# Kernel optimization log

Hardware: AMD Instinct MI355X
Metric: run time of the kernel (lower is better)

## Reference

```python
import jax, jax.numpy as jnp
import numpy as np

N_EMBD = 1024
HEAD_SIZE = 64
T = 8192
LN_EPS = 1e-5


def _layer_norm(x, gamma, beta):
    mu = jnp.mean(x, axis=-1, keepdims=True)
    var = jnp.mean(jnp.square(x - mu), axis=-1, keepdims=True)
    return (x - mu) * jax.lax.rsqrt(var + LN_EPS) * gamma + beta


def setup_inputs() -> dict:
    key = jax.random.key(0)
    ks = jax.random.split(key, 10)
    s_in = 1.0 / np.sqrt(N_EMBD)
    s_hs = 1.0 / np.sqrt(HEAD_SIZE)
    s_ff = 1.0 / np.sqrt(4 * N_EMBD)
    return {
        "x": jax.random.normal(ks[0], (T, N_EMBD), dtype=jnp.float32),
        "Wk": jax.random.uniform(ks[1], (N_EMBD, HEAD_SIZE), jnp.float32, -s_in, s_in),
        "Wq": jax.random.uniform(ks[2], (N_EMBD, HEAD_SIZE), jnp.float32, -s_in, s_in),
        "Wv": jax.random.uniform(ks[3], (N_EMBD, HEAD_SIZE), jnp.float32, -s_in, s_in),
        "Wp": jax.random.uniform(ks[4], (HEAD_SIZE, N_EMBD), jnp.float32, -s_hs, s_hs),
        "W1": jax.random.uniform(ks[5], (N_EMBD, 4 * N_EMBD), jnp.float32, -s_in, s_in),
        "b1": jax.random.uniform(ks[6], (4 * N_EMBD,), jnp.float32, -s_in, s_in),
        "W2": jax.random.uniform(ks[7], (4 * N_EMBD, N_EMBD), jnp.float32, -s_ff, s_ff),
        "b2": jax.random.uniform(ks[8], (N_EMBD,), jnp.float32, -s_ff, s_ff),
        "g1": jnp.ones((N_EMBD,), jnp.float32),
        "be1": jnp.zeros((N_EMBD,), jnp.float32),
        "g2": jnp.ones((N_EMBD,), jnp.float32),
        "be2": jnp.zeros((N_EMBD,), jnp.float32),
    }


def reference(x, Wk, Wq, Wv, Wp, W1, b1, W2, b2, g1, be1, g2, be2):
    Tn = x.shape[0]
    k = x @ Wk            # (T, hs)
    q = x @ Wq            # (T, hs)
    v = x @ Wv            # (T, hs)
    wei = (q @ k.T) * (HEAD_SIZE ** -0.5)       # (T, T)
    causal = jnp.tril(jnp.ones((Tn, Tn), dtype=bool))
    wei = jnp.where(causal, wei, -jnp.inf)
    wei = jax.nn.softmax(wei, axis=-1)
    attn = (wei @ v) @ Wp                        # (T, n_embd)
    x1 = _layer_norm(x + attn, g1, be1)
    y = jax.nn.relu(x1 @ W1 + b1) @ W2 + b2      # FFN
    return _layer_norm(x1 + y, g2, be2)
```

## Files before the change

kernel.cpp:

```cpp
#include <hip/hip_runtime.h>
#include <hip/hip_bf16.h>

#define T_SEQ 8192
#define NE 1024
#define FF 4096

typedef __bf16 bf16_t;
typedef __bf16 bf16x8 __attribute__((ext_vector_type(8)));
typedef __bf16 bf16x4 __attribute__((ext_vector_type(4)));
typedef float f32x4 __attribute__((ext_vector_type(4)));

__device__ __forceinline__ void gll16(const void* g, void* l) {
    __builtin_amdgcn_global_load_lds(
        (const __attribute__((address_space(1))) void*)g,
        (__attribute__((address_space(3))) void*)l, 16, 0, 0);
}

__global__ __launch_bounds__(256) void cast_f32_bf16(const float* __restrict__ in,
                                                     bf16_t* __restrict__ out, int n4) {
    int i = blockIdx.x * 256 + threadIdx.x;
    if (i >= n4) return;
    float4 v = ((const float4*)in)[i];
    bf16x4 h;
    h[0] = (bf16_t)v.x; h[1] = (bf16_t)v.y; h[2] = (bf16_t)v.z; h[3] = (bf16_t)v.w;
    ((bf16x4*)out)[i] = h;
}

__global__ __launch_bounds__(256) void build_wkqv(const float* __restrict__ Wk,
                                                  const float* __restrict__ Wq,
                                                  const float* __restrict__ Wv,
                                                  bf16_t* __restrict__ out) {
    int idx = blockIdx.x * 256 + threadIdx.x;
    int n  = idx >> 10;
    int kk = idx & 1023;
    float v = 0.f;
    if (n < 64)       v = Wk[kk * 64 + n];
    else if (n < 128) v = Wq[kk * 64 + (n - 64)] * 0.125f;
    else if (n < 192) v = Wv[kk * 64 + (n - 128)];
    out[idx] = (bf16_t)v;
}

__global__ __launch_bounds__(256) void tcast(const float* __restrict__ in,
                                             bf16_t* __restrict__ out, int R, int C) {
    __shared__ bf16_t tl[64][66];
    const int bc = blockIdx.x << 6, br = blockIdx.y << 6;
    const int tx = threadIdx.x & 63, ty = threadIdx.x >> 6;
#pragma unroll
    for (int j = 0; j < 16; ++j) {
        const int r = ty + j * 4;
        tl[r][tx] = (bf16_t)in[(size_t)(br + r) * C + bc + tx];
    }
    __syncthreads();
#pragma unroll
    for (int j = 0; j < 16; ++j) {
        const int r = ty + j * 4;
        out[(size_t)(bc + r) * R + br + tx] = tl[tx][r];
    }
}

template <int EPI>
__global__ __launch_bounds__(256, 2)
void gemm_bt(const bf16_t* __restrict__ A, const bf16_t* __restrict__ Bt,
             int M, int N, int K,
             float* __restrict__ outf,
             bf16_t* __restrict__ ob0, bf16_t* __restrict__ ob1, bf16_t* __restrict__ ob2,
             const float* __restrict__ res, const float* __restrict__ bias) {
    const int tid  = threadIdx.x;
    const int lane = tid & 63;
    const int tiles_n = N >> 7;
    const int tm = blockIdx.x / tiles_n;
    const int tn = blockIdx.x % tiles_n;
    const int brow = tm << 7, bcol = tn << 7;

    __shared__ __align__(16) bf16_t As[128 * 32];
    __shared__ __align__(16) bf16_t Bs[128 * 32];

    const int c1 = tid, c2 = tid + 256;
    const int s1 = (((c1 & 3) ^ ((c1 >> 3) & 3)) * 8);
    const int s2 = (((c2 & 3) ^ ((c2 >> 3) & 3)) * 8);
    const bf16_t* gA1 = A + (size_t)(brow + (c1 >> 2)) * K + s1;
    const bf16_t* gA2 = A + (size_t)(brow + (c2 >> 2)) * K + s2;
    const bf16_t* gB1 = Bt + (size_t)(bcol + (c1 >> 2)) * K + s1;
    const bf16_t* gB2 = Bt + (size_t)(bcol + (c2 >> 2)) * K + s2;
    bf16_t* lA1 = As + c1 * 8; bf16_t* lA2 = As + c2 * 8;
    bf16_t* lB1 = Bs + c1 * 8; bf16_t* lB2 = Bs + c2 * 8;

    const int wv = tid >> 6;
    const int wr = (wv >> 1) * 64, wc = (wv & 1) * 64;
    const int arow  = wr + (lane & 15);
    const int brf   = wc + (lane & 15);
    const int koff = (((lane >> 4) ^ ((lane >> 1) & 3)) * 8);

    f32x4 acc[4][4];
#pragma unroll
    for (int i = 0; i < 4; ++i)
#pragma unroll
        for (int j = 0; j < 4; ++j) acc[i][j] = (f32x4){0.f, 0.f, 0.f, 0.f};

    for (int k0 = 0; k0 < K; k0 += 32) {
        gll16(gA1, lA1); gll16(gA2, lA2);
        gll16(gB1, lB1); gll16(gB2, lB2);
        gA1 += 32; gA2 += 32; gB1 += 32; gB2 += 32;
        __syncthreads();
        bf16x8 af[4], bfr[4];
#pragma unroll
        for (int mi = 0; mi < 4; ++mi)
            af[mi] = *(const bf16x8*)(As + (arow + mi * 16) * 32 + koff);
#pragma unroll
        for (int ni = 0; ni < 4; ++ni)
            bfr[ni] = *(const bf16x8*)(Bs + (brf + ni * 16) * 32 + koff);
#pragma unroll
        for (int mi = 0; mi < 4; ++mi)
#pragma unroll
            for (int ni = 0; ni < 4; ++ni)
                acc[mi][ni] = __builtin_amdgcn_mfma_f32_16x16x32_bf16(
                    af[mi], bfr[ni], acc[mi][ni], 0, 0, 0);
        __syncthreads();
    }

    const int r0 = brow + wr + ((lane >> 4) << 2);
    const int c0 = bcol + wc + (lane & 15);
#pragma unroll
    for (int mi = 0; mi < 4; ++mi)
#pragma unroll
        for (int ni = 0; ni < 4; ++ni)
#pragma unroll
            for (int r = 0; r < 4; ++r) {
                const int row = r0 + mi * 16 + r;
                const int col = c0 + ni * 16;
                const float v = acc[mi][ni][r];
                if constexpr (EPI == 0) {
                    if (col < 64)       ob0[row * 64 + col] = (bf16_t)v;
                    else if (col < 128) ob1[row * 64 + (col - 64)] = (bf16_t)v;
                    else if (col < 192) ob2[(size_t)(col - 128) * T_SEQ + row] = (bf16_t)v;
                } else if constexpr (EPI == 1) {
                    outf[(size_t)row * N + col] = res[(size_t)row * N + col] + v;
                } else if constexpr (EPI == 2) {
                    ob0[(size_t)row * N + col] = (bf16_t)fmaxf(v + bias[col], 0.f);
                } else {
                    outf[(size_t)row * N + col] = res[(size_t)row * N + col] + v + bias[col];
                }
            }
}

template <int EPI>
__global__ __launch_bounds__(512, 1)
void gemm_ls(const bf16_t* __restrict__ A, int lda,
             const bf16_t* __restrict__ Bt, int ldb,
             int N, int K,
             bf16_t* __restrict__ ob, const float* __restrict__ bias,
             float* __restrict__ po0, float* __restrict__ po1) {
    __shared__ __align__(16) bf16_t sA[4][8192];
    __shared__ __align__(16) bf16_t sB[4][8192];
    const int tid = threadIdx.x, lane = tid & 63, w = tid >> 6;
    const int wm = w >> 2, wn = w & 3;

    const int nwg = gridDim.x;
    const int wgid = (blockIdx.x & 7) * (nwg >> 3) + (blockIdx.x >> 3);
    const int tiles_n = N >> 8;
    const int tm = wgid / tiles_n, tn = wgid % tiles_n;
    const int brow = tm << 8, bcol = tn << 8;
    const size_t kofs = (size_t)blockIdx.y * K;

    const int s0 = (w & 1) * 2, rbb = w >> 1;
    const bf16_t* gA0 = A + (size_t)(brow + rbb * 64 + lane) * lda + kofs + s0 * 8;
    const bf16_t* gB0 = Bt + (size_t)(bcol + rbb * 64 + lane) * ldb + kofs + s0 * 8;
    const int dA0 = s0 * 2048 + (rbb * 64 + lane) * 8;

    const int l15 = lane & 15, sq = lane >> 4;
    const int aoff = sq * 2048 + (wm * 128 + l15) * 8;
    const int boff = sq * 2048 + (wn * 64 + l15) * 8;
    const int NTS = K >> 5;

    f32x4 acc[8][4];
#pragma unroll
    for (int i = 0; i < 8; ++i)
#pragma unroll
        for (int j = 0; j < 4; ++j) acc[i][j] = (f32x4){0.f, 0.f, 0.f, 0.f};
    bf16x8 af[8], bfr[4];

#define L_SB  __builtin_amdgcn_sched_barrier(0)
#define L_BAR { L_SB; __builtin_amdgcn_s_barrier(); L_SB; }
#define L_LG0 { asm volatile("s_waitcnt lgkmcnt(0)" ::: "memory"); L_SB; }
#define L_VM4 { asm volatile("s_waitcnt vmcnt(4)" ::: "memory"); L_SB; }
#define L_VM0 { asm volatile("s_waitcnt vmcnt(0)" ::: "memory"); L_SB; }
#define L_STAGE(t) { const int q_ = (t) & 3; \
    gll16(gA0 + (size_t)(t) * 32,        &sA[q_][dA0]); \
    gll16(gA0 + (size_t)(t) * 32 + 8,    &sA[q_][dA0 + 2048]); \
    gll16(gB0 + (size_t)(t) * 32,        &sB[q_][dA0]); \
    gll16(gB0 + (size_t)(t) * 32 + 8,    &sB[q_][dA0 + 2048]); \
    L_SB; }
#define L_DS(t) { const int q_ = (t) & 3; \
    _Pragma("unroll") for (int m = 0; m < 8; ++m) \
        af[m] = *(const bf16x8*)(&sA[q_][aoff + m * 128]); \
    _Pragma("unroll") for (int n = 0; n < 4; ++n) \
        bfr[n] = *(const bf16x8*)(&sB[q_][boff + n * 128]); }
#define L_MMA() { __builtin_amdgcn_s_setprio(1); \
    _Pragma("unroll") for (int m = 0; m < 8; ++m) \
    _Pragma("unroll") for (int n = 0; n < 4; ++n) \
        acc[m][n] = __builtin_amdgcn_mfma_f32_16x16x32_bf16(af[m], bfr[n], acc[m][n], 0, 0, 0); \
    __builtin_amdgcn_s_setprio(0); }

    L_STAGE(0); L_STAGE(1);
    L_VM4; L_BAR;
    for (int t = 0; t < NTS - 2; ++t) {
        L_DS(t);
        L_STAGE(t + 2);
        L_LG0;
        L_MMA();
        L_VM4; L_BAR;
    }
    L_DS(NTS - 2); L_LG0; L_MMA(); L_VM0; L_BAR;
    L_DS(NTS - 1); L_LG0; L_MMA();

#undef L_MMA
#undef L_DS
#undef L_STAGE
#undef L_VM0
#undef L_VM4
#undef L_LG0
#undef L_BAR
#undef L_SB

    const int r0 = brow + wm * 128 + sq * 4;
    const int c0 = bcol + wn * 64 + l15;
    float* po = blockIdx.y ? po1 : po0;
#pragma unroll
    for (int m = 0; m < 8; ++m)
#pragma unroll
        for (int n = 0; n < 4; ++n) {
            const int col = c0 + n * 16;
#pragma unroll
            for (int r = 0; r < 4; ++r) {
                const int row = r0 + m * 16 + r;
                const float v = acc[m][n][r];
                if constexpr (EPI == 2) {
                    ob[(size_t)row * N + col] = (bf16_t)fmaxf(v + bias[col], 0.f);
                } else {
                    po[(size_t)row * N + col] = v;
                }
            }
        }
}

__global__ __launch_bounds__(256)
void attn_partial(const bf16_t* __restrict__ Q, const bf16_t* __restrict__ Kb,
                  const bf16_t* __restrict__ VT,
                  float* __restrict__ po, float* __restrict__ pml) {
    const int tid = threadIdx.x, lane = tid & 63, w = tid >> 6;
    const int j = blockIdx.x * 4 + w;

    int a = 0;
    while (j >= 16 * (a + 1) * (a + 2)) ++a;
    const int r_in = j - 16 * a * (a + 1);
    const int idx = r_in / (a + 1);
    const int chunk = r_in - idx * (a + 1);
    const int g = a * 8 + (idx >> 2);
    const int qi = g * 4 + (idx & 3);
    const int G = g >> 1;

    __shared__ __align__(16) bf16_t P[4][16 * 128];
    const int l15 = lane & 15, hi = lane >> 4;
    const int koff = hi * 8;
    const int qrow = qi * 16 + l15;
    const bf16x8 qf0 = *(const bf16x8*)(Q + qrow * 64 + koff);
    const bf16x8 qf1 = *(const bf16x8*)(Q + qrow * 64 + 32 + koff);

    float m_run[4], l_run[4];
    f32x4 oacc[4];
#pragma unroll
    for (int r = 0; r < 4; ++r) { m_run[r] = -1e30f; l_run[r] = 0.f; }
#pragma unroll
    for (int d = 0; d < 4; ++d) oacc[d] = (f32x4){0.f, 0.f, 0.f, 0.f};

    const int t0 = chunk * 4;
    const int t1 = min(t0 + 4, G + 1);
    for (int t = t0; t < t1; ++t) {
        const int kv0 = t << 7;
        f32x4 s[8];
#pragma unroll
        for (int ni = 0; ni < 8; ++ni) s[ni] = (f32x4){0.f, 0.f, 0.f, 0.f};
#pragma unroll
        for (int ni = 0; ni < 8; ++ni) {
            const bf16_t* kp = Kb + (size_t)(kv0 + ni * 16 + l15) * 64 + koff;
            bf16x8 kf0 = *(const bf16x8*)(kp);
            bf16x8 kf1 = *(const bf16x8*)(kp + 32);
            s[ni] = __builtin_amdgcn_mfma_f32_16x16x32_bf16(qf0, kf0, s[ni], 0, 0, 0);
            s[ni] = __builtin_amdgcn_mfma_f32_16x16x32_bf16(qf1, kf1, s[ni], 0, 0, 0);
        }
        if (t == G) {
#pragma unroll
            for (int ni = 0; ni < 8; ++ni)
#pragma unroll
                for (int r = 0; r < 4; ++r) {
                    const int col = kv0 + ni * 16 + l15;
                    const int row = qi * 16 + hi * 4 + r;
                    if (col > row) s[ni][r] = -1e30f;
                }
        }
        float alpha[4];
#pragma unroll
        for (int r = 0; r < 4; ++r) {
            float vm = fmaxf(fmaxf(fmaxf(s[0][r], s[1][r]), fmaxf(s[2][r], s[3][r])),
                             fmaxf(fmaxf(s[4][r], s[5][r]), fmaxf(s[6][r], s[7][r])));
            vm = fmaxf(vm, __shfl_xor(vm, 1));
            vm = fmaxf(vm, __shfl_xor(vm, 2));
            vm = fmaxf(vm, __shfl_xor(vm, 4));
            vm = fmaxf(vm, __shfl_xor(vm, 8));
            const float mnew = fmaxf(m_run[r], vm);
            float sum = 0.f;
#pragma unroll
            for (int ni = 0; ni < 8; ++ni) {
                const float p = __expf(s[ni][r] - mnew);
                s[ni][r] = p;
                sum += p;
            }
            sum += __shfl_xor(sum, 1); sum += __shfl_xor(sum, 2);
            sum += __shfl_xor(sum, 4); sum += __shfl_xor(sum, 8);
            alpha[r] = __expf(m_run[r] - mnew);
            l_run[r] = l_run[r] * alpha[r] + sum;
            m_run[r] = mnew;
        }
#pragma unroll
        for (int d = 0; d < 4; ++d)
#pragma unroll
            for (int r = 0; r < 4; ++r) oacc[d][r] *= alpha[r];
        asm volatile("s_waitcnt lgkmcnt(0)" ::: "memory");
        __builtin_amdgcn_sched_barrier(0);
#pragma unroll
        for (int ni = 0; ni < 8; ++ni)
#pragma unroll
            for (int r = 0; r < 4; ++r)
                P[w][(hi * 4 + r) * 128 + ni * 16 + l15] = (bf16_t)s[ni][r];
        asm volatile("s_waitcnt lgkmcnt(0)" ::: "memory");
        __builtin_amdgcn_sched_barrier(0);
#pragma unroll
        for (int ks = 0; ks < 4; ++ks) {
            bf16x8 pf = *(const bf16x8*)(&P[w][l15 * 128 + ks * 32 + koff]);
#pragma unroll
            for (int d = 0; d < 4; ++d) {
                bf16x8 vf = *(const bf16x8*)(VT + (size_t)(d * 16 + l15) * T_SEQ + kv0 + ks * 32 + koff);
                oacc[d] = __builtin_amdgcn_mfma_f32_16x16x32_bf16(pf, vf, oacc[d], 0, 0, 0);
            }
        }
    }
#pragma unroll
    for (int d = 0; d < 4; ++d)
#pragma unroll
        for (int r = 0; r < 4; ++r)
            po[(size_t)j * 1024 + (hi * 4 + r) * 64 + d * 16 + l15] = oacc[d][r];
    if (l15 == 0) {
#pragma unroll
        for (int r = 0; r < 4; ++r) {
            pml[(size_t)j * 32 + hi * 4 + r] = m_run[r];
            pml[(size_t)j * 32 + 16 + hi * 4 + r] = l_run[r];
        }
    }
}

__global__ __launch_bounds__(256)
void attn_reduce(const float* __restrict__ po, const float* __restrict__ pml,
                 bf16_t* __restrict__ O) {
    const int qi = blockIdx.x;
    const int tid = threadIdx.x;
    const int row = tid >> 4;
    const int cg = tid & 15;
    const int g = qi >> 2;
    const int a = g >> 3;
    const int idx = ((g & 7) << 2) | (qi & 3);
    const int base = 16 * a * (a + 1) + idx * (a + 1);
    const int cnt = a + 1;

    float M = -1e30f;
    for (int i = 0; i < cnt; ++i)
        M = fmaxf(M, pml[(size_t)(base + i) * 32 + row]);
    float L = 0.f;
    f32x4 o = (f32x4){0.f, 0.f, 0.f, 0.f};
    for (int i = 0; i < cnt; ++i) {
        const float m = pml[(size_t)(base + i) * 32 + row];
        const float l = pml[(size_t)(base + i) * 32 + 16 + row];
        const float wgt = __expf(m - M);
        L += l * wgt;
        const f32x4 v = *(const f32x4*)&po[(size_t)(base + i) * 1024 + row * 64 + cg * 4];
#pragma unroll
        for (int u = 0; u < 4; ++u) o[u] += v[u] * wgt;
    }
    const float inv = 1.f / L;
    bf16x4 h;
#pragma unroll
    for (int u = 0; u < 4; ++u) h[u] = (bf16_t)(o[u] * inv);
    *(bf16x4*)(O + (size_t)(qi * 16 + row) * 64 + cg * 4) = h;
}

__global__ __launch_bounds__(256)
void ln_fused(const float* __restrict__ in, const float* __restrict__ g,
              const float* __restrict__ b, float* __restrict__ o32,
              bf16_t* __restrict__ o16) {
    const int row = blockIdx.x, tid = threadIdx.x;
    const float4 v = ((const float4*)(in + (size_t)row * NE))[tid];
    float s = v.x + v.y + v.z + v.w;
    float ss = v.x * v.x + v.y * v.y + v.z * v.z + v.w * v.w;
#pragma unroll
    for (int off = 1; off < 64; off <<= 1) {
        s  += __shfl_xor(s, off);
        ss += __shfl_xor(ss, off);
    }
    __shared__ float red[8];
    const int wv = tid >> 6, lane = tid & 63;
    if (lane == 0) { red[wv] = s; red[4 + wv] = ss; }
    __syncthreads();
    s  = red[0] + red[1] + red[2] + red[3];
    ss = red[4] + red[5] + red[6] + red[7];
    const float mu = s * (1.f / NE);
    const float rstd = rsqrtf(ss * (1.f / NE) - mu * mu + 1e-5f);
    const float4 gg = ((const float4*)g)[tid];
    const float4 bb = ((const float4*)b)[tid];
    float4 o;
    o.x = (v.x - mu) * rstd * gg.x + bb.x;
    o.y = (v.y - mu) * rstd * gg.y + bb.y;
    o.z = (v.z - mu) * rstd * gg.z + bb.z;
    o.w = (v.w - mu) * rstd * gg.w + bb.w;
    if (o32) ((float4*)(o32 + (size_t)row * NE))[tid] = o;
    if (o16) {
        bf16x4 h;
        h[0] = (bf16_t)o.x; h[1] = (bf16_t)o.y; h[2] = (bf16_t)o.z; h[3] = (bf16_t)o.w;
        *(bf16x4*)(o16 + (size_t)row * NE + tid * 4) = h;
    }
}

__global__ __launch_bounds__(256)
void ln_sum(const float* __restrict__ r1, const float* __restrict__ p0,
            const float* __restrict__ p1, const float* __restrict__ bias,
            const float* __restrict__ g, const float* __restrict__ b,
            float* __restrict__ out) {
    const int row = blockIdx.x, tid = threadIdx.x;
    const size_t off = (size_t)row * NE;
    const float4 a = ((const float4*)(r1 + off))[tid];
    const float4 q0 = ((const float4*)(p0 + off))[tid];
    const float4 q1 = ((const float4*)(p1 + off))[tid];
    const float4 bb4 = ((const float4*)bias)[tid];
    float4 v;
    v.x = a.x + q0.x + q1.x + bb4.x;
    v.y = a.y + q0.y + q1.y + bb4.y;
    v.z = a.z + q0.z + q1.z + bb4.z;
    v.w = a.w + q0.w + q1.w + bb4.w;
    float s = v.x + v.y + v.z + v.w;
    float ss = v.x * v.x + v.y * v.y + v.z * v.z + v.w * v.w;
#pragma unroll
    for (int off2 = 1; off2 < 64; off2 <<= 1) {
        s  += __shfl_xor(s, off2);
        ss += __shfl_xor(ss, off2);
    }
    __shared__ float red[8];
    const int wv = tid >> 6, lane = tid & 63;
    if (lane == 0) { red[wv] = s; red[4 + wv] = ss; }
    __syncthreads();
    s  = red[0] + red[1] + red[2] + red[3];
    ss = red[4] + red[5] + red[6] + red[7];
    const float mu = s * (1.f / NE);
    const float rstd = rsqrtf(ss * (1.f / NE) - mu * mu + 1e-5f);
    const float4 gg = ((const float4*)g)[tid];
    const float4 be = ((const float4*)b)[tid];
    float4 o;
    o.x = (v.x - mu) * rstd * gg.x + be.x;
    o.y = (v.y - mu) * rstd * gg.y + be.y;
    o.z = (v.z - mu) * rstd * gg.z + be.z;
    o.w = (v.w - mu) * rstd * gg.w + be.w;
    ((float4*)(out + off))[tid] = o;
}

extern "C" void kernel_launch(void* const* d_in, const int* in_sizes, int n_in,
                              void* d_out, int out_size, void* d_ws, size_t ws_size,
                              hipStream_t stream) {
    (void)in_sizes; (void)n_in; (void)out_size; (void)ws_size;
    const float* x   = (const float*)d_in[0];
    const float* Wk  = (const float*)d_in[1];
    const float* Wq  = (const float*)d_in[2];
    const float* Wv  = (const float*)d_in[3];
    const float* Wp  = (const float*)d_in[4];
    const float* W1  = (const float*)d_in[5];
    const float* b1  = (const float*)d_in[6];
    const float* W2  = (const float*)d_in[7];
    const float* b2  = (const float*)d_in[8];
    const float* g1  = (const float*)d_in[9];
    const float* be1 = (const float*)d_in[10];
    const float* g2  = (const float*)d_in[11];
    const float* be2 = (const float*)d_in[12];
    float* out = (float*)d_out;

    char* ws = (char*)d_ws;
    bf16_t* xb   = (bf16_t*)(ws);
    bf16_t* x1b  = (bf16_t*)(ws + 16777216);
    bf16_t* hb   = (bf16_t*)(ws + 33554432);
    float*  po   = (float*)(ws + 33554432);
    float*  pml  = (float*)(ws + 33554432 + 18874368);
    bf16_t* W1t  = (bf16_t*)(ws + 100663296);
    bf16_t* W2t  = (bf16_t*)(ws + 109051904);
    bf16_t* Wkqv = (bf16_t*)(ws + 117440512);
    bf16_t* WpT  = (bf16_t*)(ws + 117964800);
    bf16_t* kb   = (bf16_t*)(ws + 118095872);
    bf16_t* qb   = (bf16_t*)(ws + 119144448);
    bf16_t* vT   = (bf16_t*)(ws + 120193024);
    bf16_t* a0   = (bf16_t*)(ws + 121241600);
    float*  r1   = (float*)(ws + 122290176);
    float*  pk0  = (float*)(ws + 155844608);
    float*  pk1  = (float*)(ws);

    cast_f32_bf16<<<8192, 256, 0, stream>>>(x, xb, 2097152);
    build_wkqv<<<1024, 256, 0, stream>>>(Wk, Wq, Wv, Wkqv);
    tcast<<<dim3(16, 1), 256, 0, stream>>>(Wp, WpT, 64, 1024);
    tcast<<<dim3(64, 16), 256, 0, stream>>>(W1, W1t, 1024, 4096);
    tcast<<<dim3(16, 64), 256, 0, stream>>>(W2, W2t, 4096, 1024);

    gemm_bt<0><<<64 * 2, 256, 0, stream>>>(xb, Wkqv, 8192, 256, 1024,
                                           nullptr, kb, qb, vT, nullptr, nullptr);
    attn_partial<<<1088, 256, 0, stream>>>(qb, kb, vT, po, pml);
    attn_reduce<<<512, 256, 0, stream>>>(po, pml, a0);
    gemm_bt<1><<<64 * 8, 256, 0, stream>>>(a0, WpT, 8192, 1024, 64,
                                           r1, nullptr, nullptr, nullptr, x, nullptr);
    ln_fused<<<8192, 256, 0, stream>>>(r1, g1, be1, r1, x1b);
    gemm_ls<2><<<dim3(512, 1), 512, 0, stream>>>(x1b, 1024, W1t, 1024, 4096, 1024,
                                                 hb, b1, nullptr, nullptr);
    gemm_ls<4><<<dim3(128, 2), 512, 0, stream>>>(hb, 4096, W2t, 4096, 1024, 2048,
                                                 nullptr, nullptr, pk0, pk1);
    ln_sum<<<8192, 256, 0, stream>>>(r1, pk0, pk1, b2, g2, be2, out);
}
```

Before: 348.1 us.

## Use 4-wave 128x128-per-wave FFN GEMM kernel and prefetch V in attention

Adds a new gemm_w128 kernel for the two FFN GEMMs. It uses 256 threads (4 waves), each computing a 128x128 sub-tile instead of 128x64, which raises MFMA work per LDS fragment load. LDS B-fragment reads are split into chunks with partial lgkmcnt waits so MFMAs can start before all fragments arrive. The attention PV loop now software-prefetches the next V fragments from global memory before issuing the current MFMAs. Doubling the accumulators increases register pressure and halves the waves per block, which may reduce latency hiding.

```diff
diff --git a/kernel.cpp b/kernel.cpp
--- a/kernel.cpp
+++ b/kernel.cpp
@@ -154,31 +154,26 @@
     __shared__ __align__(16) bf16_t sB[4][8192];
     const int tid = threadIdx.x, lane = tid & 63, w = tid >> 6;
     const int wm = w >> 2, wn = w & 3;
-
     const int nwg = gridDim.x;
     const int wgid = (blockIdx.x & 7) * (nwg >> 3) + (blockIdx.x >> 3);
     const int tiles_n = N >> 8;
     const int tm = wgid / tiles_n, tn = wgid % tiles_n;
     const int brow = tm << 8, bcol = tn << 8;
     const size_t kofs = (size_t)blockIdx.y * K;
-
     const int s0 = (w & 1) * 2, rbb = w >> 1;
     const bf16_t* gA0 = A + (size_t)(brow + rbb * 64 + lane) * lda + kofs + s0 * 8;
     const bf16_t* gB0 = Bt + (size_t)(bcol + rbb * 64 + lane) * ldb + kofs + s0 * 8;
     const int dA0 = s0 * 2048 + (rbb * 64 + lane) * 8;
-
     const int l15 = lane & 15, sq = lane >> 4;
     const int aoff = sq * 2048 + (wm * 128 + l15) * 8;
     const int boff = sq * 2048 + (wn * 64 + l15) * 8;
     const int NTS = K >> 5;
-
     f32x4 acc[8][4];
 #pragma unroll
     for (int i = 0; i < 8; ++i)
 #pragma unroll
         for (int j = 0; j < 4; ++j) acc[i][j] = (f32x4){0.f, 0.f, 0.f, 0.f};
     bf16x8 af[8], bfr[4];
-
 #define L_SB  __builtin_amdgcn_sched_barrier(0)
 #define L_BAR { L_SB; __builtin_amdgcn_s_barrier(); L_SB; }
 #define L_LG0 { asm volatile("s_waitcnt lgkmcnt(0)" ::: "memory"); L_SB; }
@@ -200,7 +195,6 @@
     _Pragma("unroll") for (int n = 0; n < 4; ++n) \
         acc[m][n] = __builtin_amdgcn_mfma_f32_16x16x32_bf16(af[m], bfr[n], acc[m][n], 0, 0, 0); \
     __builtin_amdgcn_s_setprio(0); }
-
     L_STAGE(0); L_STAGE(1);
     L_VM4; L_BAR;
     for (int t = 0; t < NTS - 2; ++t) {
@@ -212,7 +206,6 @@
     }
     L_DS(NTS - 2); L_LG0; L_MMA(); L_VM0; L_BAR;
     L_DS(NTS - 1); L_LG0; L_MMA();
-
 #undef L_MMA
 #undef L_DS
 #undef L_STAGE
@@ -221,7 +214,6 @@
 #undef L_LG0
 #undef L_BAR
 #undef L_SB
-
     const int r0 = brow + wm * 128 + sq * 4;
     const int c0 = bcol + wn * 64 + l15;
     float* po = blockIdx.y ? po1 : po0;
@@ -229,6 +221,120 @@
     for (int m = 0; m < 8; ++m)
 #pragma unroll
         for (int n = 0; n < 4; ++n) {
+            const int col = c0 + n * 16;
+#pragma unroll
+            for (int r = 0; r < 4; ++r) {
+                const int row = r0 + m * 16 + r;
+                const float v = acc[m][n][r];
+                if constexpr (EPI == 2) {
+                    ob[(size_t)row * N + col] = (bf16_t)fmaxf(v + bias[col], 0.f);
+                } else {
+                    po[(size_t)row * N + col] = v;
+                }
+            }
+        }
+}
+
+template <int EPI>
+__global__ __launch_bounds__(256, 1)
+void gemm_w128(const bf16_t* __restrict__ A, int lda,
+               const bf16_t* __restrict__ Bt, int ldb,
+               int N, int K,
+               bf16_t* __restrict__ ob, const float* __restrict__ bias,
+               float* __restrict__ po0, float* __restrict__ po1) {
+    __shared__ __align__(16) bf16_t sA[4][8192];
+    __shared__ __align__(16) bf16_t sB[4][8192];
+    const int tid = threadIdx.x, lane = tid & 63, w = tid >> 6;
+    const int wm = w >> 1, wn = w & 1;
+
+    const int nwg = gridDim.x;
+    const int wgid = (blockIdx.x & 7) * (nwg >> 3) + (blockIdx.x >> 3);
+    const int tiles_n = N >> 8;
+    const int tm = wgid / tiles_n, tn = wgid % tiles_n;
+    const int brow = tm << 8, bcol = tn << 8;
+    const size_t kofs = (size_t)blockIdx.y * K;
+
+    const bf16_t* gA0 = A + (size_t)(brow + lane) * lda + kofs + w * 8;
+    const bf16_t* gB0 = Bt + (size_t)(bcol + lane) * ldb + kofs + w * 8;
+    const int dst0 = w * 2048 + lane * 8;
+
+    const int l15 = lane & 15, sq = lane >> 4;
+    const int abase = sq * 2048 + (wm * 128 + l15) * 8;
+    const int bbase = sq * 2048 + (wn * 128 + l15) * 8;
+    const int NTS = K >> 5;
+
+    f32x4 acc[8][8];
+#pragma unroll
+    for (int i = 0; i < 8; ++i)
+#pragma unroll
+        for (int j = 0; j < 8; ++j) acc[i][j] = (f32x4){0.f, 0.f, 0.f, 0.f};
+    bf16x8 af[8], bf[8];
+
+#define W_SB  __builtin_amdgcn_sched_barrier(0)
+#define W_BAR { W_SB; __builtin_amdgcn_s_barrier(); W_SB; }
+#define W_LGK(n) { asm volatile("s_waitcnt lgkmcnt(" #n ")" ::: "memory"); W_SB; }
+#define W_VM8 { asm volatile("s_waitcnt vmcnt(8)" ::: "memory"); W_SB; }
+#define W_VM0 { asm volatile("s_waitcnt vmcnt(0)" ::: "memory"); W_SB; }
+#define W_STAGE(t) { const int q_ = (t) & 3; \
+    _Pragma("unroll") for (int rb = 0; rb < 4; ++rb) \
+        gll16(gA0 + (size_t)(rb * 64) * lda + (size_t)(t) * 32, &sA[q_][dst0 + rb * 512]); \
+    _Pragma("unroll") for (int rb = 0; rb < 4; ++rb) \
+        gll16(gB0 + (size_t)(rb * 64) * ldb + (size_t)(t) * 32, &sB[q_][dst0 + rb * 512]); \
+    W_SB; }
+#define W_ISSUE(t) { const int q_ = (t) & 3; \
+    _Pragma("unroll") for (int m = 0; m < 8; ++m) \
+        af[m] = *(const bf16x8*)(&sA[q_][abase + m * 128]); \
+    bf[0] = *(const bf16x8*)(&sB[q_][bbase]); \
+    bf[1] = *(const bf16x8*)(&sB[q_][bbase + 128]); \
+    W_SB; \
+    bf[2] = *(const bf16x8*)(&sB[q_][bbase + 256]); \
+    bf[3] = *(const bf16x8*)(&sB[q_][bbase + 384]); \
+    W_SB; \
+    bf[4] = *(const bf16x8*)(&sB[q_][bbase + 512]); \
+    bf[5] = *(const bf16x8*)(&sB[q_][bbase + 640]); \
+    W_SB; \
+    bf[6] = *(const bf16x8*)(&sB[q_][bbase + 768]); \
+    bf[7] = *(const bf16x8*)(&sB[q_][bbase + 896]); \
+    W_SB; }
+#define W_MMA2(n0) { __builtin_amdgcn_s_setprio(1); \
+    _Pragma("unroll") for (int m = 0; m < 8; ++m) { \
+        acc[m][n0] = __builtin_amdgcn_mfma_f32_16x16x32_bf16(af[m], bf[n0], acc[m][n0], 0, 0, 0); \
+        acc[m][n0 + 1] = __builtin_amdgcn_mfma_f32_16x16x32_bf16(af[m], bf[n0 + 1], acc[m][n0 + 1], 0, 0, 0); } \
+    __builtin_amdgcn_s_setprio(0); }
+#define W_CHUNKS { W_LGK(6); W_MMA2(0); W_LGK(4); W_MMA2(2); \
+                   W_LGK(2); W_MMA2(4); W_LGK(0); W_MMA2(6); }
+
+    W_STAGE(0); W_STAGE(1);
+    W_VM8; W_BAR;
+    for (int t = 0; t < NTS - 2; ++t) {
+        W_ISSUE(t);
+        W_STAGE(t + 2);
+        W_CHUNKS;
+        W_VM8; W_BAR;
+    }
+    W_ISSUE(NTS - 2);
+    W_CHUNKS;
+    W_VM0; W_BAR;
+    W_ISSUE(NTS - 1);
+    W_CHUNKS;
+
+#undef W_CHUNKS
+#undef W_MMA2
+#undef W_ISSUE
+#undef W_STAGE
+#undef W_VM0
+#undef W_VM8
+#undef W_LGK
+#undef W_BAR
+#undef W_SB
+
+    const int r0 = brow + wm * 128 + sq * 4;
+    const int c0 = bcol + wn * 128 + l15;
+    float* po = blockIdx.y ? po1 : po0;
+#pragma unroll
+    for (int m = 0; m < 8; ++m)
+#pragma unroll
+        for (int n = 0; n < 8; ++n) {
             const int col = c0 + n * 16;
 #pragma unroll
             for (int r = 0; r < 4; ++r) {
@@ -325,6 +431,10 @@
         for (int d = 0; d < 4; ++d)
 #pragma unroll
             for (int r = 0; r < 4; ++r) oacc[d][r] *= alpha[r];
+        bf16x8 vcur[4], vnxt[4];
+#pragma unroll
+        for (int d = 0; d < 4; ++d)
+            vcur[d] = *(const bf16x8*)(VT + (size_t)(d * 16 + l15) * T_SEQ + kv0 + koff);
         asm volatile("s_waitcnt lgkmcnt(0)" ::: "memory");
         __builtin_amdgcn_sched_barrier(0);
 #pragma unroll
@@ -337,11 +447,17 @@
 #pragma unroll
         for (int ks = 0; ks < 4; ++ks) {
             bf16x8 pf = *(const bf16x8*)(&P[w][l15 * 128 + ks * 32 + koff]);
-#pragma unroll
-            for (int d = 0; d < 4; ++d) {
-                bf16x8 vf = *(const bf16x8*)(VT + (size_t)(d * 16 + l15) * T_SEQ + kv0 + ks * 32 + koff);
-                oacc[d] = __builtin_amdgcn_mfma_f32_16x16x32_bf16(pf, vf, oacc[d], 0, 0, 0);
+            if (ks < 3) {
+#pragma unroll
+                for (int d = 0; d < 4; ++d)
+                    vnxt[d] = *(const bf16x8*)(VT + (size_t)(d * 16 + l15) * T_SEQ +
+                                               kv0 + (ks + 1) * 32 + koff);
             }
+#pragma unroll
+            for (int d = 0; d < 4; ++d)
+                oacc[d] = __builtin_amdgcn_mfma_f32_16x16x32_bf16(pf, vcur[d], oacc[d], 0, 0, 0);
+#pragma unroll
+            for (int d = 0; d < 4; ++d) vcur[d] = vnxt[d];
         }
     }
 #pragma unroll
@@ -519,9 +635,9 @@
     gemm_bt<1><<<64 * 8, 256, 0, stream>>>(a0, WpT, 8192, 1024, 64,
                                            r1, nullptr, nullptr, nullptr, x, nullptr);
     ln_fused<<<8192, 256, 0, stream>>>(r1, g1, be1, r1, x1b);
-    gemm_ls<2><<<dim3(512, 1), 512, 0, stream>>>(x1b, 1024, W1t, 1024, 4096, 1024,
-                                                 hb, b1, nullptr, nullptr);
-    gemm_ls<4><<<dim3(128, 2), 512, 0, stream>>>(hb, 4096, W2t, 4096, 1024, 2048,
-                                                 nullptr, nullptr, pk0, pk1);
+    gemm_w128<2><<<dim3(512, 1), 256, 0, stream>>>(x1b, 1024, W1t, 1024, 4096, 1024,
+                                                   hb, b1, nullptr, nullptr);
+    gemm_w128<4><<<dim3(128, 2), 256, 0, stream>>>(hb, 4096, W2t, 4096, 1024, 2048,
+                                                   nullptr, nullptr, pk0, pk1);
     ln_sum<<<8192, 256, 0, stream>>>(r1, pk0, pk1, b2, g2, be2, out);
 }
```

New measurement: 413.1 us. +18.7%, slower.

## Add 256x128-tile GEMM for FFN up-projection and prefetch V in attention

Applied to the files above, without the earlier changes.

Adds a gemm_bn128 kernel with 256x128 output tiles, a 3-stage LDS ring and launch bounds that allow 2 workgroups per CU. It replaces gemm_ls for the W1 GEMM, which now runs on 1024 workgroups instead of 512. The goal is better occupancy and latency hiding, at the cost of less operand reuse per tile. Separately, the attention PV loop now software-pipelines the V global loads one k-step ahead to hide their latency, which uses more registers.

```diff
diff --git a/kernel.cpp b/kernel.cpp
--- a/kernel.cpp
+++ b/kernel.cpp
@@ -154,31 +154,26 @@
     __shared__ __align__(16) bf16_t sB[4][8192];
     const int tid = threadIdx.x, lane = tid & 63, w = tid >> 6;
     const int wm = w >> 2, wn = w & 3;
-
     const int nwg = gridDim.x;
     const int wgid = (blockIdx.x & 7) * (nwg >> 3) + (blockIdx.x >> 3);
     const int tiles_n = N >> 8;
     const int tm = wgid / tiles_n, tn = wgid % tiles_n;
     const int brow = tm << 8, bcol = tn << 8;
     const size_t kofs = (size_t)blockIdx.y * K;
-
     const int s0 = (w & 1) * 2, rbb = w >> 1;
     const bf16_t* gA0 = A + (size_t)(brow + rbb * 64 + lane) * lda + kofs + s0 * 8;
     const bf16_t* gB0 = Bt + (size_t)(bcol + rbb * 64 + lane) * ldb + kofs + s0 * 8;
     const int dA0 = s0 * 2048 + (rbb * 64 + lane) * 8;
-
     const int l15 = lane & 15, sq = lane >> 4;
     const int aoff = sq * 2048 + (wm * 128 + l15) * 8;
     const int boff = sq * 2048 + (wn * 64 + l15) * 8;
     const int NTS = K >> 5;
-
     f32x4 acc[8][4];
 #pragma unroll
     for (int i = 0; i < 8; ++i)
 #pragma unroll
         for (int j = 0; j < 4; ++j) acc[i][j] = (f32x4){0.f, 0.f, 0.f, 0.f};
     bf16x8 af[8], bfr[4];
-
 #define L_SB  __builtin_amdgcn_sched_barrier(0)
 #define L_BAR { L_SB; __builtin_amdgcn_s_barrier(); L_SB; }
 #define L_LG0 { asm volatile("s_waitcnt lgkmcnt(0)" ::: "memory"); L_SB; }
@@ -200,7 +195,6 @@
     _Pragma("unroll") for (int n = 0; n < 4; ++n) \
         acc[m][n] = __builtin_amdgcn_mfma_f32_16x16x32_bf16(af[m], bfr[n], acc[m][n], 0, 0, 0); \
     __builtin_amdgcn_s_setprio(0); }
-
     L_STAGE(0); L_STAGE(1);
     L_VM4; L_BAR;
     for (int t = 0; t < NTS - 2; ++t) {
@@ -212,7 +206,6 @@
     }
     L_DS(NTS - 2); L_LG0; L_MMA(); L_VM0; L_BAR;
     L_DS(NTS - 1); L_LG0; L_MMA();
-
 #undef L_MMA
 #undef L_DS
 #undef L_STAGE
@@ -221,12 +214,113 @@
 #undef L_LG0
 #undef L_BAR
 #undef L_SB
-
     const int r0 = brow + wm * 128 + sq * 4;
     const int c0 = bcol + wn * 64 + l15;
     float* po = blockIdx.y ? po1 : po0;
 #pragma unroll
     for (int m = 0; m < 8; ++m)
+#pragma unroll
+        for (int n = 0; n < 4; ++n) {
+            const int col = c0 + n * 16;
+#pragma unroll
+            for (int r = 0; r < 4; ++r) {
+                const int row = r0 + m * 16 + r;
+                const float v = acc[m][n][r];
+                if constexpr (EPI == 2) {
+                    ob[(size_t)row * N + col] = (bf16_t)fmaxf(v + bias[col], 0.f);
+                } else {
+                    po[(size_t)row * N + col] = v;
+                }
+            }
+        }
+}
+
+template <int EPI>
+__global__ __launch_bounds__(512, 2)
+void gemm_bn128(const bf16_t* __restrict__ A, int lda,
+                const bf16_t* __restrict__ Bt, int ldb,
+                int N, int K,
+                bf16_t* __restrict__ ob, const float* __restrict__ bias,
+                float* __restrict__ po0, float* __restrict__ po1) {
+    __shared__ __align__(16) bf16_t sA[3][8192];
+    __shared__ __align__(16) bf16_t sB[3][4096];
+    const int tid = threadIdx.x, lane = tid & 63, w = tid >> 6;
+    const int wm = w >> 1, wn = w & 1;
+
+    const int nwg = gridDim.x;
+    const int wgid = (blockIdx.x & 7) * (nwg >> 3) + (blockIdx.x >> 3);
+    const int tiles_n = N >> 7;
+    const int tm = wgid / tiles_n, tn = wgid % tiles_n;
+    const int brow = tm << 8, bcol = tn << 7;
+    const size_t kofs = (size_t)blockIdx.y * K;
+
+    const int cA0 = w * 2, cA1 = w * 2 + 1;
+    const bf16_t* gA_0 = A + (size_t)(brow + (cA0 >> 2) * 64 + lane) * lda + kofs + (cA0 & 3) * 8;
+    const bf16_t* gA_1 = A + (size_t)(brow + (cA1 >> 2) * 64 + lane) * lda + kofs + (cA1 & 3) * 8;
+    const int dA_0 = (cA0 & 3) * 2048 + ((cA0 >> 2) * 64 + lane) * 8;
+    const int dA_1 = (cA1 & 3) * 2048 + ((cA1 >> 2) * 64 + lane) * 8;
+    const bf16_t* gB_0 = Bt + (size_t)(bcol + (w >> 2) * 64 + lane) * ldb + kofs + (w & 3) * 8;
+    const int dB_0 = (w & 3) * 1024 + ((w >> 2) * 64 + lane) * 8;
+
+    const int l15 = lane & 15, sq = lane >> 4;
+    const int aoff = sq * 2048 + (wm * 64 + l15) * 8;
+    const int boff = sq * 1024 + (wn * 64 + l15) * 8;
+    const int NTS = K >> 5;
+
+    f32x4 acc[4][4];
+#pragma unroll
+    for (int i = 0; i < 4; ++i)
+#pragma unroll
+        for (int j = 0; j < 4; ++j) acc[i][j] = (f32x4){0.f, 0.f, 0.f, 0.f};
+    bf16x8 af[4], bfr[4];
+
+#define N_SB  __builtin_amdgcn_sched_barrier(0)
+#define N_BAR { N_SB; __builtin_amdgcn_s_barrier(); N_SB; }
+#define N_LG0 { asm volatile("s_waitcnt lgkmcnt(0)" ::: "memory"); N_SB; }
+#define N_VM3 { asm volatile("s_waitcnt vmcnt(3)" ::: "memory"); N_SB; }
+#define N_VM0 { asm volatile("s_waitcnt vmcnt(0)" ::: "memory"); N_SB; }
+#define N_STAGE(t) { const int q_ = (t) % 3; \
+    gll16(gA_0 + (size_t)(t) * 32, &sA[q_][dA_0]); \
+    gll16(gA_1 + (size_t)(t) * 32, &sA[q_][dA_1]); \
+    gll16(gB_0 + (size_t)(t) * 32, &sB[q_][dB_0]); \
+    N_SB; }
+#define N_DS(t) { const int q_ = (t) % 3; \
+    _Pragma("unroll") for (int m = 0; m < 4; ++m) \
+        af[m] = *(const bf16x8*)(&sA[q_][aoff + m * 128]); \
+    _Pragma("unroll") for (int n = 0; n < 4; ++n) \
+        bfr[n] = *(const bf16x8*)(&sB[q_][boff + n * 128]); }
+#define N_MMA() { __builtin_amdgcn_s_setprio(1); \
+    _Pragma("unroll") for (int m = 0; m < 4; ++m) \
+    _Pragma("unroll") for (int n = 0; n < 4; ++n) \
+        acc[m][n] = __builtin_amdgcn_mfma_f32_16x16x32_bf16(af[m], bfr[n], acc[m][n], 0, 0, 0); \
+    __builtin_amdgcn_s_setprio(0); }
+
+    N_STAGE(0); N_STAGE(1);
+    N_VM3; N_BAR;
+    for (int t = 0; t < NTS - 2; ++t) {
+        N_DS(t);
+        N_STAGE(t + 2);
+        N_LG0;
+        N_MMA();
+        N_VM3; N_BAR;
+    }
+    N_DS(NTS - 2); N_LG0; N_MMA(); N_VM0; N_BAR;
+    N_DS(NTS - 1); N_LG0; N_MMA();
+
+#undef N_MMA
+#undef N_DS
+#undef N_STAGE
+#undef N_VM0
+#undef N_VM3
+#undef N_LG0
+#undef N_BAR
+#undef N_SB
+
+    const int r0 = brow + wm * 64 + (sq << 2);
+    const int c0 = bcol + wn * 64 + l15;
+    float* po = blockIdx.y ? po1 : po0;
+#pragma unroll
+    for (int m = 0; m < 4; ++m)
 #pragma unroll
         for (int n = 0; n < 4; ++n) {
             const int col = c0 + n * 16;
@@ -325,6 +419,10 @@
         for (int d = 0; d < 4; ++d)
 #pragma unroll
             for (int r = 0; r < 4; ++r) oacc[d][r] *= alpha[r];
+        bf16x8 vcur[4], vnxt[4];
+#pragma unroll
+        for (int d = 0; d < 4; ++d)
+            vcur[d] = *(const bf16x8*)(VT + (size_t)(d * 16 + l15) * T_SEQ + kv0 + koff);
         asm volatile("s_waitcnt lgkmcnt(0)" ::: "memory");
         __builtin_amdgcn_sched_barrier(0);
 #pragma unroll
@@ -337,11 +435,17 @@
 #pragma unroll
         for (int ks = 0; ks < 4; ++ks) {
             bf16x8 pf = *(const bf16x8*)(&P[w][l15 * 128 + ks * 32 + koff]);
-#pragma unroll
-            for (int d = 0; d < 4; ++d) {
-                bf16x8 vf = *(const bf16x8*)(VT + (size_t)(d * 16 + l15) * T_SEQ + kv0 + ks * 32 + koff);
-                oacc[d] = __builtin_amdgcn_mfma_f32_16x16x32_bf16(pf, vf, oacc[d], 0, 0, 0);
+            if (ks < 3) {
+#pragma unroll
+                for (int d = 0; d < 4; ++d)
+                    vnxt[d] = *(const bf16x8*)(VT + (size_t)(d * 16 + l15) * T_SEQ +
+                                               kv0 + (ks + 1) * 32 + koff);
             }
+#pragma unroll
+            for (int d = 0; d < 4; ++d)
+                oacc[d] = __builtin_amdgcn_mfma_f32_16x16x32_bf16(pf, vcur[d], oacc[d], 0, 0, 0);
+#pragma unroll
+            for (int d = 0; d < 4; ++d) vcur[d] = vnxt[d];
         }
     }
 #pragma unroll
@@ -519,8 +623,8 @@
     gemm_bt<1><<<64 * 8, 256, 0, stream>>>(a0, WpT, 8192, 1024, 64,
                                            r1, nullptr, nullptr, nullptr, x, nullptr);
     ln_fused<<<8192, 256, 0, stream>>>(r1, g1, be1, r1, x1b);
-    gemm_ls<2><<<dim3(512, 1), 512, 0, stream>>>(x1b, 1024, W1t, 1024, 4096, 1024,
-                                                 hb, b1, nullptr, nullptr);
+    gemm_bn128<2><<<dim3(1024, 1), 512, 0, stream>>>(x1b, 1024, W1t, 1024, 4096, 1024,
+                                                     hb, b1, nullptr, nullptr);
     gemm_ls<4><<<dim3(128, 2), 512, 0, stream>>>(hb, 4096, W2t, 4096, 1024, 2048,
                                                  nullptr, nullptr, pk0, pk1);
     ln_sum<<<8192, 256, 0, stream>>>(r1, pk0, pk1, b2, g2, be2, out);
```

After: 389.9 us. +12.0%, slower.

## Add K=64 double-buffered GEMM with chunked LDS-wait interleaving for FFN up-projection

Applied to the files above, without the earlier changes.

Adds a new gemm_k64 kernel that stages 64-wide K slices in two LDS buffers instead of 32-wide slices in four. It issues all LDS fragment reads up front and waits on them in chunks with staged lgkmcnt counts, so MFMA work on early fragments overlaps the remaining LDS reads. The W1 GEMM now launches this kernel, halving the number of barrier iterations per tile. The trade-off is shallower global prefetch depth (double instead of quadruple buffering) and a vmcnt(0) wait every iteration, which may expose global load latency.

```diff
diff --git a/kernel.cpp b/kernel.cpp
--- a/kernel.cpp
+++ b/kernel.cpp
@@ -154,31 +154,26 @@
     __shared__ __align__(16) bf16_t sB[4][8192];
     const int tid = threadIdx.x, lane = tid & 63, w = tid >> 6;
     const int wm = w >> 2, wn = w & 3;
-
     const int nwg = gridDim.x;
     const int wgid = (blockIdx.x & 7) * (nwg >> 3) + (blockIdx.x >> 3);
     const int tiles_n = N >> 8;
     const int tm = wgid / tiles_n, tn = wgid % tiles_n;
     const int brow = tm << 8, bcol = tn << 8;
     const size_t kofs = (size_t)blockIdx.y * K;
-
     const int s0 = (w & 1) * 2, rbb = w >> 1;
     const bf16_t* gA0 = A + (size_t)(brow + rbb * 64 + lane) * lda + kofs + s0 * 8;
     const bf16_t* gB0 = Bt + (size_t)(bcol + rbb * 64 + lane) * ldb + kofs + s0 * 8;
     const int dA0 = s0 * 2048 + (rbb * 64 + lane) * 8;
-
     const int l15 = lane & 15, sq = lane >> 4;
     const int aoff = sq * 2048 + (wm * 128 + l15) * 8;
     const int boff = sq * 2048 + (wn * 64 + l15) * 8;
     const int NTS = K >> 5;
-
     f32x4 acc[8][4];
 #pragma unroll
     for (int i = 0; i < 8; ++i)
 #pragma unroll
         for (int j = 0; j < 4; ++j) acc[i][j] = (f32x4){0.f, 0.f, 0.f, 0.f};
     bf16x8 af[8], bfr[4];
-
 #define L_SB  __builtin_amdgcn_sched_barrier(0)
 #define L_BAR { L_SB; __builtin_amdgcn_s_barrier(); L_SB; }
 #define L_LG0 { asm volatile("s_waitcnt lgkmcnt(0)" ::: "memory"); L_SB; }
@@ -200,7 +195,6 @@
     _Pragma("unroll") for (int n = 0; n < 4; ++n) \
         acc[m][n] = __builtin_amdgcn_mfma_f32_16x16x32_bf16(af[m], bfr[n], acc[m][n], 0, 0, 0); \
     __builtin_amdgcn_s_setprio(0); }
-
     L_STAGE(0); L_STAGE(1);
     L_VM4; L_BAR;
     for (int t = 0; t < NTS - 2; ++t) {
@@ -212,7 +206,6 @@
     }
     L_DS(NTS - 2); L_LG0; L_MMA(); L_VM0; L_BAR;
     L_DS(NTS - 1); L_LG0; L_MMA();
-
 #undef L_MMA
 #undef L_DS
 #undef L_STAGE
@@ -221,6 +214,125 @@
 #undef L_LG0
 #undef L_BAR
 #undef L_SB
+    const int r0 = brow + wm * 128 + sq * 4;
+    const int c0 = bcol + wn * 64 + l15;
+    float* po = blockIdx.y ? po1 : po0;
+#pragma unroll
+    for (int m = 0; m < 8; ++m)
+#pragma unroll
+        for (int n = 0; n < 4; ++n) {
+            const int col = c0 + n * 16;
+#pragma unroll
+            for (int r = 0; r < 4; ++r) {
+                const int row = r0 + m * 16 + r;
+                const float v = acc[m][n][r];
+                if constexpr (EPI == 2) {
+                    ob[(size_t)row * N + col] = (bf16_t)fmaxf(v + bias[col], 0.f);
+                } else {
+                    po[(size_t)row * N + col] = v;
+                }
+            }
+        }
+}
+
+template <int EPI>
+__global__ __launch_bounds__(512, 1)
+void gemm_k64(const bf16_t* __restrict__ A, int lda,
+              const bf16_t* __restrict__ Bt, int ldb,
+              int N, int K,
+              bf16_t* __restrict__ ob, const float* __restrict__ bias,
+              float* __restrict__ po0, float* __restrict__ po1) {
+    __shared__ __align__(16) bf16_t sA[2][16384];
+    __shared__ __align__(16) bf16_t sB[2][16384];
+    const int tid = threadIdx.x, lane = tid & 63, w = tid >> 6;
+    const int wm = w >> 2, wn = w & 3;
+
+    const int nwg = gridDim.x;
+    const int wgid = (blockIdx.x & 7) * (nwg >> 3) + (blockIdx.x >> 3);
+    const int tiles_n = N >> 8;
+    const int tm = wgid / tiles_n, tn = wgid % tiles_n;
+    const int brow = tm << 8, bcol = tn << 8;
+    const size_t kofs = (size_t)blockIdx.y * K;
+
+    const bf16_t* gA0 = A + (size_t)(brow + lane) * lda + kofs + w * 8;
+    const bf16_t* gB0 = Bt + (size_t)(bcol + lane) * ldb + kofs + w * 8;
+    const int dst0 = w * 2048 + lane * 8;
+
+    const int l15 = lane & 15, sq = lane >> 4;
+    const int arow8 = (wm * 128 + l15) * 8;
+    const int brow8 = (wn * 64 + l15) * 8;
+    const int NTS = K >> 6;
+
+    f32x4 acc[8][4];
+#pragma unroll
+    for (int i = 0; i < 8; ++i)
+#pragma unroll
+        for (int j = 0; j < 4; ++j) acc[i][j] = (f32x4){0.f, 0.f, 0.f, 0.f};
+    bf16x8 af[8][2], bfr[4][2];
+
+#define K_SB  __builtin_amdgcn_sched_barrier(0)
+#define K_BAR { K_SB; __builtin_amdgcn_s_barrier(); K_SB; }
+#define K_LGK(n) { asm volatile("s_waitcnt lgkmcnt(" #n ")" ::: "memory"); K_SB; }
+#define K_VM0 { asm volatile("s_waitcnt vmcnt(0)" ::: "memory"); K_SB; }
+#define K_STAGE(t) { const int q_ = (t) & 1; \
+    _Pragma("unroll") for (int rb = 0; rb < 4; ++rb) \
+        gll16(gA0 + (size_t)(rb * 64) * lda + (size_t)(t) * 64, &sA[q_][dst0 + rb * 512]); \
+    _Pragma("unroll") for (int rb = 0; rb < 4; ++rb) \
+        gll16(gB0 + (size_t)(rb * 64) * ldb + (size_t)(t) * 64, &sB[q_][dst0 + rb * 512]); \
+    K_SB; }
+#define K_ISSUE(t) { const int q_ = (t) & 1; \
+    _Pragma("unroll") for (int n = 0; n < 4; ++n) { \
+        bfr[n][0] = *(const bf16x8*)(&sB[q_][sq * 2048 + brow8 + n * 128]); \
+        bfr[n][1] = *(const bf16x8*)(&sB[q_][(4 + sq) * 2048 + brow8 + n * 128]); } \
+    K_SB; \
+    af[0][0] = *(const bf16x8*)(&sA[q_][sq * 2048 + arow8]); \
+    af[0][1] = *(const bf16x8*)(&sA[q_][(4 + sq) * 2048 + arow8]); \
+    af[1][0] = *(const bf16x8*)(&sA[q_][sq * 2048 + arow8 + 128]); \
+    af[1][1] = *(const bf16x8*)(&sA[q_][(4 + sq) * 2048 + arow8 + 128]); \
+    K_SB; \
+    af[2][0] = *(const bf16x8*)(&sA[q_][sq * 2048 + arow8 + 256]); \
+    af[2][1] = *(const bf16x8*)(&sA[q_][(4 + sq) * 2048 + arow8 + 256]); \
+    af[3][0] = *(const bf16x8*)(&sA[q_][sq * 2048 + arow8 + 384]); \
+    af[3][1] = *(const bf16x8*)(&sA[q_][(4 + sq) * 2048 + arow8 + 384]); \
+    K_SB; \
+    af[4][0] = *(const bf16x8*)(&sA[q_][sq * 2048 + arow8 + 512]); \
+    af[4][1] = *(const bf16x8*)(&sA[q_][(4 + sq) * 2048 + arow8 + 512]); \
+    af[5][0] = *(const bf16x8*)(&sA[q_][sq * 2048 + arow8 + 640]); \
+    af[5][1] = *(const bf16x8*)(&sA[q_][(4 + sq) * 2048 + arow8 + 640]); \
+    K_SB; \
+    af[6][0] = *(const bf16x8*)(&sA[q_][sq * 2048 + arow8 + 768]); \
+    af[6][1] = *(const bf16x8*)(&sA[q_][(4 + sq) * 2048 + arow8 + 768]); \
+    af[7][0] = *(const bf16x8*)(&sA[q_][sq * 2048 + arow8 + 896]); \
+    af[7][1] = *(const bf16x8*)(&sA[q_][(4 + sq) * 2048 + arow8 + 896]); \
+    K_SB; }
+#define K_MMA2(m0) { __builtin_amdgcn_s_setprio(1); \
+    _Pragma("unroll") for (int mm = (m0); mm < (m0) + 2; ++mm) \
+    _Pragma("unroll") for (int ks = 0; ks < 2; ++ks) \
+    _Pragma("unroll") for (int n = 0; n < 4; ++n) \
+        acc[mm][n] = __builtin_amdgcn_mfma_f32_16x16x32_bf16(af[mm][ks], bfr[n][ks], acc[mm][n], 0, 0, 0); \
+    __builtin_amdgcn_s_setprio(0); }
+#define K_CHUNKS { K_LGK(12); K_MMA2(0); K_LGK(8); K_MMA2(2); \
+                   K_LGK(4); K_MMA2(4); K_LGK(0); K_MMA2(6); }
+
+    K_STAGE(0);
+    K_VM0; K_BAR;
+    for (int t = 0; t < NTS - 1; ++t) {
+        K_ISSUE(t);
+        K_STAGE(t + 1);
+        K_CHUNKS;
+        K_VM0; K_BAR;
+    }
+    K_ISSUE(NTS - 1);
+    K_CHUNKS;
+
+#undef K_CHUNKS
+#undef K_MMA2
+#undef K_ISSUE
+#undef K_STAGE
+#undef K_VM0
+#undef K_LGK
+#undef K_BAR
+#undef K_SB
 
     const int r0 = brow + wm * 128 + sq * 4;
     const int c0 = bcol + wn * 64 + l15;
@@ -519,8 +631,8 @@
     gemm_bt<1><<<64 * 8, 256, 0, stream>>>(a0, WpT, 8192, 1024, 64,
                                            r1, nullptr, nullptr, nullptr, x, nullptr);
     ln_fused<<<8192, 256, 0, stream>>>(r1, g1, be1, r1, x1b);
-    gemm_ls<2><<<dim3(512, 1), 512, 0, stream>>>(x1b, 1024, W1t, 1024, 4096, 1024,
-                                                 hb, b1, nullptr, nullptr);
+    gemm_k64<2><<<dim3(512, 1), 512, 0, stream>>>(x1b, 1024, W1t, 1024, 4096, 1024,
+                                                  hb, b1, nullptr, nullptr);
     gemm_ls<4><<<dim3(128, 2), 512, 0, stream>>>(hb, 4096, W2t, 4096, 1024, 2048,
                                                  nullptr, nullptr, pk0, pk1);
     ln_sum<<<8192, 256, 0, stream>>>(r1, pk0, pk1, b2, g2, be2, out);
```

After: 357.7 us. 2.8% more time.
